# Optimization experiments

Measured on AMD Instinct MI355X. Metric: run time of the kernel, lower is better.

## Reference

```python
import jax, jax.numpy as jnp
import numpy as np

B, S, D = 2, 2048, 2048
NH, NKV, HD = 16, 4, 128
ROPE_BASE = 10000.0
NEG = -1e9


def _rope_tables(seq_len, dim):
    inv_freq = 1.0 / ROPE_BASE ** (jnp.arange(0, dim, 2, dtype=jnp.float32) / dim)
    t = jnp.arange(seq_len, dtype=jnp.float32)
    freqs = jnp.outer(t, inv_freq)                      # [S, dim/2]
    return jnp.cos(freqs), jnp.sin(freqs)


def _apply_rope(x, cos, sin):
    # x: [B, S, H, HD]; interleaved-pair rotation matching the original module
    x1 = x[..., ::2]
    x2 = x[..., 1::2]
    c = cos[None, :, None, :]
    s = sin[None, :, None, :]
    out1 = x1 * c - x2 * s
    out2 = x1 * s + x2 * c
    return jnp.stack([out1, out2], axis=-1).reshape(x.shape)


def setup_inputs() -> dict:
    key = jax.random.key(0)
    ks = jax.random.split(key, 5)
    x = jax.random.normal(ks[0], (B, S, D), dtype=jnp.float32)
    # causal additive mask [1, 1, S, S]
    causal = jnp.tril(jnp.ones((S, S), dtype=jnp.bool_))
    mask = jnp.where(causal, 0.0, NEG).astype(jnp.float32)[None, None]
    Wq = jax.random.normal(ks[1], (D, NH * HD), dtype=jnp.float32) * (D ** -0.5)
    Wk = jax.random.normal(ks[2], (D, NKV * HD), dtype=jnp.float32) * (D ** -0.5)
    Wv = jax.random.normal(ks[3], (D, NKV * HD), dtype=jnp.float32) * (D ** -0.5)
    Wo = jax.random.normal(ks[4], (NH * HD, D), dtype=jnp.float32) * ((NH * HD) ** -0.5)
    return {"x": x, "mask": mask, "Wq": Wq, "Wk": Wk, "Wv": Wv, "Wo": Wo}


def reference(x, mask, Wq, Wk, Wv, Wo):
    b, s, _ = x.shape
    q = (x @ Wq).reshape(b, s, NH, HD)
    k = (x @ Wk).reshape(b, s, NKV, HD)
    v = (x @ Wv).reshape(b, s, NKV, HD)

    cos, sin = _rope_tables(s, HD)
    q = _apply_rope(q, cos, sin)
    k = _apply_rope(k, cos, sin)

    rep = NH // NKV
    k = jnp.repeat(k, rep, axis=2)                       # [b, s, NH, HD]
    v = jnp.repeat(v, rep, axis=2)

    q = q.transpose(0, 2, 1, 3)                          # [b, NH, s, HD]
    k = k.transpose(0, 2, 1, 3)
    v = v.transpose(0, 2, 1, 3)

    scores = jnp.einsum('bhqd,bhkd->bhqk', q, k) / jnp.sqrt(jnp.float32(HD))
    scores = scores + mask
    attn = jax.nn.softmax(scores, axis=-1)
    out = jnp.einsum('bhqk,bhkd->bhqd', attn, v)
    out = out.transpose(0, 2, 1, 3).reshape(b, s, NH * HD)
    return out @ Wo
```

## Files before the change

### kernel.cpp

```cpp
#include <hip/hip_runtime.h>
#include <stdint.h>

#define B_    2
#define S_    2048
#define D_    2048
#define NH_   16
#define NKV_  4
#define HD_   128
#define M_    (B_*S_)
#define NQKV_ 3072

typedef __bf16 bf16x8 __attribute__((ext_vector_type(8)));
typedef float  f32x4  __attribute__((ext_vector_type(4)));

__device__ __forceinline__ unsigned short f2bf(float f) {
    unsigned int u = __float_as_uint(f);
    u += 0x7fffu + ((u >> 16) & 1u);
    return (unsigned short)(u >> 16);
}

__device__ __forceinline__ void async_cp16(const unsigned short* g, unsigned short* l) {
    __builtin_amdgcn_global_load_lds((const __attribute__((address_space(1))) void*)g,
                                     (__attribute__((address_space(3))) void*)l, 16, 0, 0);
}

__global__ void cast_x(const float* __restrict__ x, unsigned short* __restrict__ xb) {
    int idx = blockIdx.x * 256 + threadIdx.x;
    float4 v = ((const float4*)x)[idx];
    unsigned int lo = (unsigned int)f2bf(v.x) | ((unsigned int)f2bf(v.y) << 16);
    unsigned int hi = (unsigned int)f2bf(v.z) | ((unsigned int)f2bf(v.w) << 16);
    ((uint2*)xb)[idx] = make_uint2(lo, hi);
}

__global__ void transpose_cast(const float* __restrict__ src,
                               unsigned short* __restrict__ dst, int ncols) {
    __shared__ float tile[32][33];
    int tx = threadIdx.x, ty = threadIdx.y;
    int n0 = blockIdx.x * 32, k0 = blockIdx.y * 32;
#pragma unroll
    for (int i = 0; i < 4; i++) {
        int k = k0 + ty + i * 8;
        tile[ty + i * 8][tx] = src[(long)k * ncols + n0 + tx];
    }
    __syncthreads();
#pragma unroll
    for (int i = 0; i < 4; i++) {
        int n = n0 + ty + i * 8;
        dst[(long)n * 2048 + k0 + tx] = f2bf(tile[tx][ty + i * 8]);
    }
}

__global__ void rope_tables(float2* __restrict__ ctab) {
    int gid = blockIdx.x * 256 + threadIdx.x;
    int s = gid >> 6, i = gid & 63;
    float inv = exp2f(-(float)i * 0.20762050593046014f);
    float ang = (float)s * inv;
    float sn, cs; sincosf(ang, &sn, &cs);
    ctab[gid] = make_float2(cs, sn);
}

__global__ __launch_bounds__(256) void gemm_qkv(const unsigned short* __restrict__ A,
                                                const unsigned short* __restrict__ Bt,
                                                const float2* __restrict__ ctab,
                                                unsigned short* __restrict__ Qr,
                                                unsigned short* __restrict__ Kr,
                                                unsigned short* __restrict__ Vrow) {
    __shared__ unsigned short As[128 * 32];
    __shared__ unsigned short Bs[128 * 32];
    const int K = D_;
    const int bx = blockIdx.x, by = blockIdx.y;
    const int tid  = threadIdx.x;
    const int lane = tid & 63, wid = tid >> 6;
    const int quad = lane >> 4, l16 = lane & 15;
    const int wm = wid >> 1, wn = wid & 1;
    const int m0 = by * 128, n0 = bx * 128;
    f32x4 acc[4][4] = {};

    for (int k0 = 0; k0 < K; k0 += 32) {
        __syncthreads();
#pragma unroll
        for (int i = 0; i < 2; i++) {
            int gbase = (wid * 2 + i) * 64;
            int g = gbase + lane;
            int row = g >> 2, c = (g & 3) * 8;
            async_cp16(&A[(long)(m0 + row) * K + k0 + c], &As[gbase * 8]);
            async_cp16(&Bt[(long)(n0 + row) * K + k0 + c], &Bs[gbase * 8]);
        }
        __syncthreads();
        bf16x8 af[4], bfr[4];
#pragma unroll
        for (int mt = 0; mt < 4; mt++)
            af[mt] = *(const bf16x8*)&As[(wm * 64 + mt * 16 + l16) * 32 + quad * 8];
#pragma unroll
        for (int nt = 0; nt < 4; nt++)
            bfr[nt] = *(const bf16x8*)&Bs[(wn * 64 + nt * 16 + l16) * 32 + quad * 8];
#pragma unroll
        for (int mt = 0; mt < 4; mt++)
#pragma unroll
            for (int nt = 0; nt < 4; nt++)
                acc[mt][nt] = __builtin_amdgcn_mfma_f32_16x16x32_bf16(af[mt], bfr[nt], acc[mt][nt], 0, 0, 0);
    }

    if (bx < 20) {
#pragma unroll
        for (int mt = 0; mt < 4; mt++)
#pragma unroll
            for (int nt = 0; nt < 4; nt++)
#pragma unroll
                for (int r = 0; r < 4; r++) {
                    int row = m0 + wm * 64 + mt * 16 + quad * 4 + r;
                    int s = row & 2047, b = row >> 11;
                    int col = n0 + wn * 64 + nt * 16 + l16;
                    int d = col & 127;
                    float2 cs = ctab[s * 64 + (d >> 1)];
                    float own = acc[mt][nt][r];
                    float other = __shfl_xor(own, 1);
                    float val = (d & 1) ? (other * cs.y + own * cs.x)
                                        : (own * cs.x - other * cs.y);
                    if (col < 2048) {
                        int h = col >> 7;
                        Qr[(((long)(b * 16 + h) * 2048 + s) * 128) + d] = f2bf(val);
                    } else {
                        int kvh = (col - 2048) >> 7;
                        Kr[(((long)(b * 4 + kvh) * 2048 + s) * 128) + d] = f2bf(val);
                    }
                }
    } else {
#pragma unroll
        for (int mt = 0; mt < 4; mt++)
#pragma unroll
            for (int nt = 0; nt < 4; nt++)
#pragma unroll
                for (int r = 0; r < 4; r++) {
                    int row = m0 + wm * 64 + mt * 16 + quad * 4 + r;
                    int col = n0 + wn * 64 + nt * 16 + l16;
                    Vrow[(long)row * 512 + (col - 2560)] = f2bf(acc[mt][nt][r]);
                }
    }
}

__global__ __launch_bounds__(256) void gemm_bt(const unsigned short* __restrict__ A,
                                               const unsigned short* __restrict__ Bt,
                                               float* __restrict__ C, int N, int K) {
    __shared__ unsigned short As[128 * 32];
    __shared__ unsigned short Bs[128 * 32];
    const int bx = blockIdx.x, by = blockIdx.y;
    const int tid  = threadIdx.x;
    const int lane = tid & 63, wid = tid >> 6;
    const int quad = lane >> 4, l16 = lane & 15;
    const int wm = wid >> 1, wn = wid & 1;
    const int m0 = by * 128, n0 = bx * 128;
    f32x4 acc[4][4] = {};

    for (int k0 = 0; k0 < K; k0 += 32) {
        __syncthreads();
#pragma unroll
        for (int i = 0; i < 2; i++) {
            int gbase = (wid * 2 + i) * 64;
            int g = gbase + lane;
            int row = g >> 2, c = (g & 3) * 8;
            async_cp16(&A[(long)(m0 + row) * K + k0 + c], &As[gbase * 8]);
            async_cp16(&Bt[(long)(n0 + row) * K + k0 + c], &Bs[gbase * 8]);
        }
        __syncthreads();
        bf16x8 af[4], bfr[4];
#pragma unroll
        for (int mt = 0; mt < 4; mt++)
            af[mt] = *(const bf16x8*)&As[(wm * 64 + mt * 16 + l16) * 32 + quad * 8];
#pragma unroll
        for (int nt = 0; nt < 4; nt++)
            bfr[nt] = *(const bf16x8*)&Bs[(wn * 64 + nt * 16 + l16) * 32 + quad * 8];
#pragma unroll
        for (int mt = 0; mt < 4; mt++)
#pragma unroll
            for (int nt = 0; nt < 4; nt++)
                acc[mt][nt] = __builtin_amdgcn_mfma_f32_16x16x32_bf16(af[mt], bfr[nt], acc[mt][nt], 0, 0, 0);
    }
#pragma unroll
    for (int mt = 0; mt < 4; mt++)
#pragma unroll
        for (int nt = 0; nt < 4; nt++)
#pragma unroll
            for (int r = 0; r < 4; r++) {
                long row = m0 + wm * 64 + mt * 16 + quad * 4 + r;
                long col = n0 + wn * 64 + nt * 16 + l16;
                C[row * N + col] = acc[mt][nt][r];
            }
}

__global__ void v_trans_bf(const unsigned short* __restrict__ Vrow,
                           unsigned short* __restrict__ Vt) {
    __shared__ unsigned short tile[32][34];
    int tx = threadIdx.x, ty = threadIdx.y;
    int s0 = blockIdx.x * 32, d0 = blockIdx.y * 32;
    int bz = blockIdx.z;
    int b = bz >> 2, kvh = bz & 3;
#pragma unroll
    for (int i = 0; i < 4; i++) {
        int s = s0 + ty + i * 8;
        tile[ty + i * 8][tx] = Vrow[(long)(b * 2048 + s) * 512 + kvh * 128 + d0 + tx];
    }
    __syncthreads();
#pragma unroll
    for (int i = 0; i < 4; i++) {
        int d = d0 + ty + i * 8;
        Vt[((long)bz * 128 + d) * 2048 + s0 + tx] = tile[tx][ty + i * 8];
    }
}

__global__ __launch_bounds__(256) void attn_fwd(const unsigned short* __restrict__ Qr,
                                                const unsigned short* __restrict__ Kr,
                                                const unsigned short* __restrict__ Vt,
                                                unsigned short* __restrict__ O) {
    __shared__ unsigned short Ks[64][136];
    __shared__ unsigned short Vs[128][72];
    __shared__ unsigned short Ps[4][16][72];
    const int tid  = threadIdx.x;
    const int lane = tid & 63, wid = tid >> 6;
    const int quad = lane >> 4, l16 = lane & 15;
    const int pid = blockIdx.x, h = blockIdx.y, b = blockIdx.z;
    const int kvh = h >> 2;
    const unsigned short* qp = Qr + (long)(b * NH_ + h) * S_ * HD_;
    const unsigned short* kp = Kr + (long)(b * NKV_ + kvh) * S_ * HD_;
    const unsigned short* vp = Vt + (long)(b * NKV_ + kvh) * HD_ * S_;
    const float sc2 = 0.08838834764831845f * 1.4426950408889634f;

    bf16x8 ones;
#pragma unroll
    for (int i = 0; i < 8; i++) ones[i] = (__bf16)1.0f;

    for (int phase = 0; phase < 2; phase++) {
        const int qt = phase ? pid : 31 - pid;
        const int qw = qt * 64 + wid * 16;

        bf16x8 aq[4];
#pragma unroll
        for (int ks = 0; ks < 4; ks++)
            aq[ks] = *(const bf16x8*)&qp[(long)(qw + l16) * HD_ + ks * 32 + quad * 8];

        f32x4 o[8] = {};
        float mi[4], li[4];
#pragma unroll
        for (int r = 0; r < 4; r++) { mi[r] = -3.0e38f; li[r] = 0.f; }

        for (int kt = 0; kt <= qt; kt++) {
            const int kv0 = kt * 64;
            __syncthreads();
#pragma unroll
            for (int i = 0; i < 4; i++) {
                int idx = tid + i * 256;
                int row = idx >> 4, c = (idx & 15) * 8;
                *(uint4*)&Ks[row][c] = *(const uint4*)&kp[(long)(kv0 + row) * HD_ + c];
            }
#pragma unroll
            for (int i = 0; i < 4; i++) {
                int idx = tid + i * 256;
                int hd = idx >> 3, c = (idx & 7) * 8;
                *(uint4*)&Vs[hd][c] = *(const uint4*)&vp[(long)hd * S_ + kv0 + c];
            }
            __syncthreads();

            f32x4 s[4] = {};
#pragma unroll
            for (int ks = 0; ks < 4; ks++)
#pragma unroll
                for (int nt = 0; nt < 4; nt++) {
                    bf16x8 kb = *(const bf16x8*)&Ks[nt * 16 + l16][ks * 32 + quad * 8];
                    s[nt] = __builtin_amdgcn_mfma_f32_16x16x32_bf16(aq[ks], kb, s[nt], 0, 0, 0);
                }

            float mt[4];
#pragma unroll
            for (int r = 0; r < 4; r++) mt[r] = -3.0e38f;
            if (kv0 + 63 > qw) {
#pragma unroll
                for (int nt = 0; nt < 4; nt++) {
                    int kvp = kv0 + nt * 16 + l16;
#pragma unroll
                    for (int r = 0; r < 4; r++) {
                        float sv = s[nt][r] * sc2;
                        sv = (kvp <= qw + quad * 4 + r) ? sv : -1.0e30f;
                        s[nt][r] = sv;
                        mt[r] = fmaxf(mt[r], sv);
                    }
                }
            } else {
#pragma unroll
                for (int nt = 0; nt < 4; nt++)
#pragma unroll
                    for (int r = 0; r < 4; r++) {
                        float sv = s[nt][r] * sc2;
                        s[nt][r] = sv;
                        mt[r] = fmaxf(mt[r], sv);
                    }
            }
#pragma unroll
            for (int off = 1; off < 16; off <<= 1)
#pragma unroll
                for (int r = 0; r < 4; r++)
                    mt[r] = fmaxf(mt[r], __shfl_xor(mt[r], off));
            float al[4];
#pragma unroll
            for (int r = 0; r < 4; r++) {
                float mn = fmaxf(mi[r], mt[r]);
                al[r] = exp2f(mi[r] - mn);
                mi[r] = mn;
            }
#pragma unroll
            for (int nt = 0; nt < 4; nt++)
#pragma unroll
                for (int r = 0; r < 4; r++)
                    s[nt][r] = exp2f(s[nt][r] - mi[r]);
#pragma unroll
            for (int t = 0; t < 8; t++)
#pragma unroll
                for (int r = 0; r < 4; r++) o[t][r] *= al[r];

#pragma unroll
            for (int nt = 0; nt < 4; nt++)
#pragma unroll
                for (int r = 0; r < 4; r++)
                    Ps[wid][quad * 4 + r][nt * 16 + l16] = f2bf(s[nt][r]);

            f32x4 sumf = {};
#pragma unroll
            for (int ks2 = 0; ks2 < 2; ks2++) {
                bf16x8 pa = *(const bf16x8*)&Ps[wid][l16][ks2 * 32 + quad * 8];
                sumf = __builtin_amdgcn_mfma_f32_16x16x32_bf16(pa, ones, sumf, 0, 0, 0);
#pragma unroll
                for (int vt = 0; vt < 8; vt++) {
                    bf16x8 vb = *(const bf16x8*)&Vs[vt * 16 + l16][ks2 * 32 + quad * 8];
                    o[vt] = __builtin_amdgcn_mfma_f32_16x16x32_bf16(pa, vb, o[vt], 0, 0, 0);
                }
            }
#pragma unroll
            for (int r = 0; r < 4; r++) li[r] = li[r] * al[r] + sumf[r];
        }

#pragma unroll
        for (int r = 0; r < 4; r++) {
            float inv_l = 1.0f / li[r];
            int qpos = qw + quad * 4 + r;
#pragma unroll
            for (int vt = 0; vt < 8; vt++) {
                float val = o[vt][r] * inv_l;
                O[(long)(b * S_ + qpos) * 2048 + h * 128 + vt * 16 + l16] = f2bf(val);
            }
        }
    }
}

extern "C" void kernel_launch(void* const* d_in, const int* in_sizes, int n_in,
                              void* d_out, int out_size, void* d_ws, size_t ws_size,
                              hipStream_t stream) {
    const float* x  = (const float*)d_in[0];
    const float* Wq = (const float*)d_in[2];
    const float* Wk = (const float*)d_in[3];
    const float* Wv = (const float*)d_in[4];
    const float* Wo = (const float*)d_in[5];

    char* ws = (char*)d_ws;
    unsigned short* xb    = (unsigned short*)(ws);
    unsigned short* Wqkvt = (unsigned short*)(ws + 16777216);
    unsigned short* Wot   = (unsigned short*)(ws + 29360128);
    float2*         ctab  = (float2*)        (ws + 37748736);
    unsigned short* Qr    = (unsigned short*)(ws + 38797312);
    unsigned short* Kr    = (unsigned short*)(ws + 55574528);
    unsigned short* Vrow  = (unsigned short*)(ws + 59768832);
    unsigned short* Vt    = (unsigned short*)(ws + 63963136);
    unsigned short* attn  = (unsigned short*)(ws + 68157440);

    cast_x<<<8192, 256, 0, stream>>>(x, xb);
    dim3 tb(32, 8);
    transpose_cast<<<dim3(64, 64), tb, 0, stream>>>(Wq, Wqkvt, 2048);
    transpose_cast<<<dim3(16, 64), tb, 0, stream>>>(Wk, Wqkvt + 2048 * 2048, 512);
    transpose_cast<<<dim3(16, 64), tb, 0, stream>>>(Wv, Wqkvt + 2560 * 2048, 512);
    transpose_cast<<<dim3(64, 64), tb, 0, stream>>>(Wo, Wot, 2048);
    rope_tables<<<512, 256, 0, stream>>>(ctab);

    gemm_qkv<<<dim3(24, 32), 256, 0, stream>>>(xb, Wqkvt, ctab, Qr, Kr, Vrow);

    v_trans_bf<<<dim3(64, 4, 8), tb, 0, stream>>>(Vrow, Vt);

    attn_fwd<<<dim3(16, NH_, B_), 256, 0, stream>>>(Qr, Kr, Vt, attn);

    gemm_bt<<<dim3(16, 32), 256, 0, stream>>>(attn, Wot, (float*)d_out, D_, NH_ * HD_);
}
```

Baseline: 381.7 us.

## Replace 128x128 GEMMs with pipelined 256x256 tile core using swizzled LDS

Both the QKV projection and output projection GEMMs now use a shared 256x256-tile core with 8 waves and 128 KB of dynamic LDS. It prefetches K-halves asynchronously into quadrant buffers and issues MFMA clusters between barriers with raised wave priority. LDS addresses are XOR-swizzled to reduce bank conflicts. The goal is more reuse per loaded byte and overlap of global loads with matrix math. The cost is lower block count (192 and 128 blocks) and possible occupancy or tail-wave inefficiency on the CU count.

```diff
diff --git a/kernel.cpp b/kernel.cpp
--- a/kernel.cpp
+++ b/kernel.cpp
@@ -59,133 +59,270 @@
     ctab[gid] = make_float2(cs, sn);
 }
 
-__global__ __launch_bounds__(256) void gemm_qkv(const unsigned short* __restrict__ A,
-                                                const unsigned short* __restrict__ Bt,
-                                                const float2* __restrict__ ctab,
-                                                unsigned short* __restrict__ Qr,
-                                                unsigned short* __restrict__ Kr,
-                                                unsigned short* __restrict__ Vrow) {
-    __shared__ unsigned short As[128 * 32];
-    __shared__ unsigned short Bs[128 * 32];
-    const int K = D_;
-    const int bx = blockIdx.x, by = blockIdx.y;
+
+__device__ __forceinline__ bf16x8 lds_frag(const unsigned short* hb, int r, int ks, int quad) {
+    int p = (r * 128 + ks * 64 + quad * 16) ^ ((r & 4) << 3);
+    return *(const bf16x8*)((const char*)hb + p);
+}
+
+__device__ __forceinline__ void stage_half(const unsigned short* g, int Kel,
+                                           unsigned short* lhalf, int wid, int lane) {
+#pragma unroll
+    for (int i = 0; i < 2; i++) {
+        int chunk = wid * 2 + i;
+        int o = chunk * 1024 + lane * 16;
+        int row = o >> 7;
+        int cb = (o & 127) ^ ((row & 4) << 3);
+        async_cp16((const unsigned short*)((const char*)g + (size_t)row * Kel * 2 + cb),
+                   lhalf + chunk * 512);
+    }
+}
+
+template<int MB, int NB>
+__device__ __forceinline__ void cluster(f32x4 (*acc)[4], bf16x8 (*a)[2], bf16x8 (*b)[2]) {
+    __builtin_amdgcn_sched_barrier(0);
+    __builtin_amdgcn_s_barrier();
+    asm volatile("s_waitcnt lgkmcnt(0)" ::: "memory");
+    __builtin_amdgcn_sched_barrier(0);
+    __builtin_amdgcn_s_setprio(1);
+#pragma unroll
+    for (int ks = 0; ks < 2; ks++)
+#pragma unroll
+        for (int mi = 0; mi < 4; mi++)
+#pragma unroll
+            for (int ni = 0; ni < 2; ni++)
+                acc[MB + mi][NB + ni] = __builtin_amdgcn_mfma_f32_16x16x32_bf16(
+                    a[mi][ks], b[ni][ks], acc[MB + mi][NB + ni], 0, 0, 0);
+    __builtin_amdgcn_s_setprio(0);
+    __builtin_amdgcn_sched_barrier(0);
+    __builtin_amdgcn_s_barrier();
+    __builtin_amdgcn_sched_barrier(0);
+}
+
+__device__ __forceinline__ void gemm256_core(const unsigned short* __restrict__ A,
+                                             const unsigned short* __restrict__ Bt,
+                                             const int K, const int m0, const int n0,
+                                             char* sm, f32x4 (*acc)[4]) {
     const int tid  = threadIdx.x;
     const int lane = tid & 63, wid = tid >> 6;
     const int quad = lane >> 4, l16 = lane & 15;
-    const int wm = wid >> 1, wn = wid & 1;
-    const int m0 = by * 128, n0 = bx * 128;
-    f32x4 acc[4][4] = {};
-
-    for (int k0 = 0; k0 < K; k0 += 32) {
-        __syncthreads();
-#pragma unroll
-        for (int i = 0; i < 2; i++) {
-            int gbase = (wid * 2 + i) * 64;
-            int g = gbase + lane;
-            int row = g >> 2, c = (g & 3) * 8;
-            async_cp16(&A[(long)(m0 + row) * K + k0 + c], &As[gbase * 8]);
-            async_cp16(&Bt[(long)(n0 + row) * K + k0 + c], &Bs[gbase * 8]);
-        }
-        __syncthreads();
-        bf16x8 af[4], bfr[4];
-#pragma unroll
-        for (int mt = 0; mt < 4; mt++)
-            af[mt] = *(const bf16x8*)&As[(wm * 64 + mt * 16 + l16) * 32 + quad * 8];
-#pragma unroll
-        for (int nt = 0; nt < 4; nt++)
-            bfr[nt] = *(const bf16x8*)&Bs[(wn * 64 + nt * 16 + l16) * 32 + quad * 8];
-#pragma unroll
-        for (int mt = 0; mt < 4; mt++)
-#pragma unroll
-            for (int nt = 0; nt < 4; nt++)
-                acc[mt][nt] = __builtin_amdgcn_mfma_f32_16x16x32_bf16(af[mt], bfr[nt], acc[mt][nt], 0, 0, 0);
-    }
-
-    if (bx < 20) {
-#pragma unroll
-        for (int mt = 0; mt < 4; mt++)
-#pragma unroll
-            for (int nt = 0; nt < 4; nt++)
+    const int wm = wid >> 2, wn = wid & 3;
+
+    unsigned short* sA00 = (unsigned short*)(sm);
+    unsigned short* sA01 = (unsigned short*)(sm + 16384);
+    unsigned short* sA10 = (unsigned short*)(sm + 32768);
+    unsigned short* sA11 = (unsigned short*)(sm + 49152);
+    unsigned short* sB00 = (unsigned short*)(sm + 65536);
+    unsigned short* sB01 = (unsigned short*)(sm + 81920);
+    unsigned short* sB10 = (unsigned short*)(sm + 98304);
+    unsigned short* sB11 = (unsigned short*)(sm + 114688);
+
+    const unsigned short* A0 = A  + (size_t)m0 * K;
+    const unsigned short* A1 = A  + (size_t)(m0 + 128) * K;
+    const unsigned short* B0 = Bt + (size_t)n0 * K;
+    const unsigned short* B1 = Bt + (size_t)(n0 + 128) * K;
+
+    stage_half(A0,      K, sA00, wid, lane);
+    stage_half(B1,      K, sB01, wid, lane);
+    stage_half(A1,      K, sA01, wid, lane);
+    stage_half(B0,      K, sB00, wid, lane);
+    __builtin_amdgcn_sched_barrier(0);
+    stage_half(A0 + 64, K, sA10, wid, lane);
+    stage_half(B1 + 64, K, sB11, wid, lane);
+    stage_half(A1 + 64, K, sA11, wid, lane);
+    asm volatile("s_waitcnt vmcnt(6)" ::: "memory");
+    __builtin_amdgcn_sched_barrier(0);
+    __builtin_amdgcn_s_barrier();
+    __builtin_amdgcn_sched_barrier(0);
+
+    const int NIT = K >> 7;
+    for (int j = 0; j < NIT; ++j) {
+        const bool st = (j < NIT - 1);
+        const int kof1 = (2 * j + 1) * 64;
+        const int kof2 = (2 * j + 2) * 64;
+        const int kof3 = (2 * j + 3) * 64;
+        bf16x8 af[4][2], bA[2][2], bB[2][2];
+
+#pragma unroll
+        for (int mi = 0; mi < 4; mi++)
+#pragma unroll
+            for (int ks = 0; ks < 2; ks++)
+                af[mi][ks] = lds_frag(sA00, wm * 64 + mi * 16 + l16, ks, quad);
+#pragma unroll
+        for (int ni = 0; ni < 2; ni++)
+#pragma unroll
+            for (int ks = 0; ks < 2; ks++)
+                bA[ni][ks] = lds_frag(sB00, wn * 32 + ni * 16 + l16, ks, quad);
+        stage_half(B0 + kof1, K, sB10, wid, lane);
+        cluster<0, 0>(acc, af, bA);
+
+#pragma unroll
+        for (int ni = 0; ni < 2; ni++)
+#pragma unroll
+            for (int ks = 0; ks < 2; ks++)
+                bB[ni][ks] = lds_frag(sB01, wn * 32 + ni * 16 + l16, ks, quad);
+        if (st) stage_half(A0 + kof2, K, sA00, wid, lane);
+        cluster<0, 2>(acc, af, bB);
+
+#pragma unroll
+        for (int mi = 0; mi < 4; mi++)
+#pragma unroll
+            for (int ks = 0; ks < 2; ks++)
+                af[mi][ks] = lds_frag(sA01, wm * 64 + mi * 16 + l16, ks, quad);
+        if (st) stage_half(B1 + kof2, K, sB01, wid, lane);
+        cluster<4, 2>(acc, af, bB);
+
+#pragma unroll
+        for (int ni = 0; ni < 2; ni++)
+#pragma unroll
+            for (int ks = 0; ks < 2; ks++)
+                bA[ni][ks] = lds_frag(sB00, wn * 32 + ni * 16 + l16, ks, quad);
+        if (st) {
+            stage_half(A1 + kof2, K, sA01, wid, lane);
+            asm volatile("s_waitcnt vmcnt(6)" ::: "memory");
+        } else {
+            asm volatile("s_waitcnt vmcnt(0)" ::: "memory");
+        }
+        cluster<4, 0>(acc, af, bA);
+
+#pragma unroll
+        for (int mi = 0; mi < 4; mi++)
+#pragma unroll
+            for (int ks = 0; ks < 2; ks++)
+                af[mi][ks] = lds_frag(sA10, wm * 64 + mi * 16 + l16, ks, quad);
+#pragma unroll
+        for (int ni = 0; ni < 2; ni++)
+#pragma unroll
+            for (int ks = 0; ks < 2; ks++)
+                bA[ni][ks] = lds_frag(sB10, wn * 32 + ni * 16 + l16, ks, quad);
+        if (st) stage_half(B0 + kof2, K, sB00, wid, lane);
+        cluster<0, 0>(acc, af, bA);
+
+#pragma unroll
+        for (int ni = 0; ni < 2; ni++)
+#pragma unroll
+            for (int ks = 0; ks < 2; ks++)
+                bB[ni][ks] = lds_frag(sB11, wn * 32 + ni * 16 + l16, ks, quad);
+        if (st) stage_half(A0 + kof3, K, sA10, wid, lane);
+        cluster<0, 2>(acc, af, bB);
+
+#pragma unroll
+        for (int mi = 0; mi < 4; mi++)
+#pragma unroll
+            for (int ks = 0; ks < 2; ks++)
+                af[mi][ks] = lds_frag(sA11, wm * 64 + mi * 16 + l16, ks, quad);
+        if (st) stage_half(B1 + kof3, K, sB11, wid, lane);
+        cluster<4, 2>(acc, af, bB);
+
+#pragma unroll
+        for (int ni = 0; ni < 2; ni++)
+#pragma unroll
+            for (int ks = 0; ks < 2; ks++)
+                bA[ni][ks] = lds_frag(sB10, wn * 32 + ni * 16 + l16, ks, quad);
+        if (st) {
+            stage_half(A1 + kof3, K, sA11, wid, lane);
+            asm volatile("s_waitcnt vmcnt(6)" ::: "memory");
+        }
+        cluster<4, 0>(acc, af, bA);
+    }
+}
+
+__global__ __launch_bounds__(512, 2) void gemm_qkv256(const unsigned short* __restrict__ A,
+                                                      const unsigned short* __restrict__ Bt,
+                                                      const float2* __restrict__ ctab,
+                                                      unsigned short* __restrict__ Qr,
+                                                      unsigned short* __restrict__ Kr,
+                                                      unsigned short* __restrict__ Vrow) {
+    extern __shared__ char sm[];
+    const int m0 = blockIdx.y * 256, n0 = blockIdx.x * 256;
+    f32x4 acc[8][4] = {};
+    gemm256_core(A, Bt, D_, m0, n0, sm, acc);
+
+    const int tid  = threadIdx.x;
+    const int lane = tid & 63, wid = tid >> 6;
+    const int quad = lane >> 4, l16 = lane & 15;
+    const int wm = wid >> 2, wn = wid & 3;
+
+    if (n0 < 2048) {
+#pragma unroll
+        for (int mt = 0; mt < 8; mt++) {
+            int rowb = m0 + ((mt & 4) << 5) + wm * 64 + (mt & 3) * 16 + quad * 4;
+#pragma unroll
+            for (int nt = 0; nt < 4; nt++) {
+                int col = n0 + ((nt & 2) << 6) + wn * 32 + (nt & 1) * 16 + l16;
+                int h = col >> 7, d = col & 127;
 #pragma unroll
                 for (int r = 0; r < 4; r++) {
-                    int row = m0 + wm * 64 + mt * 16 + quad * 4 + r;
+                    int row = rowb + r;
                     int s = row & 2047, b = row >> 11;
-                    int col = n0 + wn * 64 + nt * 16 + l16;
-                    int d = col & 127;
                     float2 cs = ctab[s * 64 + (d >> 1)];
                     float own = acc[mt][nt][r];
                     float other = __shfl_xor(own, 1);
                     float val = (d & 1) ? (other * cs.y + own * cs.x)
                                         : (own * cs.x - other * cs.y);
-                    if (col < 2048) {
-                        int h = col >> 7;
-                        Qr[(((long)(b * 16 + h) * 2048 + s) * 128) + d] = f2bf(val);
-                    } else {
-                        int kvh = (col - 2048) >> 7;
-                        Kr[(((long)(b * 4 + kvh) * 2048 + s) * 128) + d] = f2bf(val);
-                    }
+                    Qr[((size_t)(b * 16 + h) * 2048 + s) * 128 + d] = f2bf(val);
                 }
+            }
+        }
+    } else if (n0 < 2560) {
+#pragma unroll
+        for (int mt = 0; mt < 8; mt++) {
+            int rowb = m0 + ((mt & 4) << 5) + wm * 64 + (mt & 3) * 16 + quad * 4;
+#pragma unroll
+            for (int nt = 0; nt < 4; nt++) {
+                int col = n0 + ((nt & 2) << 6) + wn * 32 + (nt & 1) * 16 + l16;
+                int kvh = (col - 2048) >> 7, d = col & 127;
+#pragma unroll
+                for (int r = 0; r < 4; r++) {
+                    int row = rowb + r;
+                    int s = row & 2047, b = row >> 11;
+                    float2 cs = ctab[s * 64 + (d >> 1)];
+                    float own = acc[mt][nt][r];
+                    float other = __shfl_xor(own, 1);
+                    float val = (d & 1) ? (other * cs.y + own * cs.x)
+                                        : (own * cs.x - other * cs.y);
+                    Kr[((size_t)(b * 4 + kvh) * 2048 + s) * 128 + d] = f2bf(val);
+                }
+            }
+        }
     } else {
 #pragma unroll
-        for (int mt = 0; mt < 4; mt++)
-#pragma unroll
-            for (int nt = 0; nt < 4; nt++)
-#pragma unroll
-                for (int r = 0; r < 4; r++) {
-                    int row = m0 + wm * 64 + mt * 16 + quad * 4 + r;
-                    int col = n0 + wn * 64 + nt * 16 + l16;
-                    Vrow[(long)row * 512 + (col - 2560)] = f2bf(acc[mt][nt][r]);
-                }
-    }
-}
-
-__global__ __launch_bounds__(256) void gemm_bt(const unsigned short* __restrict__ A,
-                                               const unsigned short* __restrict__ Bt,
-                                               float* __restrict__ C, int N, int K) {
-    __shared__ unsigned short As[128 * 32];
-    __shared__ unsigned short Bs[128 * 32];
-    const int bx = blockIdx.x, by = blockIdx.y;
+        for (int mt = 0; mt < 8; mt++) {
+            int rowb = m0 + ((mt & 4) << 5) + wm * 64 + (mt & 3) * 16 + quad * 4;
+#pragma unroll
+            for (int nt = 0; nt < 4; nt++) {
+                int col = n0 + ((nt & 2) << 6) + wn * 32 + (nt & 1) * 16 + l16;
+#pragma unroll
+                for (int r = 0; r < 4; r++)
+                    Vrow[(size_t)(rowb + r) * 512 + (col - 2560)] = f2bf(acc[mt][nt][r]);
+            }
+        }
+    }
+}
+
+__global__ __launch_bounds__(512, 2) void gemm_bt256(const unsigned short* __restrict__ A,
+                                                     const unsigned short* __restrict__ Bt,
+                                                     float* __restrict__ C) {
+    extern __shared__ char sm[];
+    const int m0 = blockIdx.y * 256, n0 = blockIdx.x * 256;
+    f32x4 acc[8][4] = {};
+    gemm256_core(A, Bt, NH_ * HD_, m0, n0, sm, acc);
+
     const int tid  = threadIdx.x;
     const int lane = tid & 63, wid = tid >> 6;
     const int quad = lane >> 4, l16 = lane & 15;
-    const int wm = wid >> 1, wn = wid & 1;
-    const int m0 = by * 128, n0 = bx * 128;
-    f32x4 acc[4][4] = {};
-
-    for (int k0 = 0; k0 < K; k0 += 32) {
-        __syncthreads();
-#pragma unroll
-        for (int i = 0; i < 2; i++) {
-            int gbase = (wid * 2 + i) * 64;
-            int g = gbase + lane;
-            int row = g >> 2, c = (g & 3) * 8;
-            async_cp16(&A[(long)(m0 + row) * K + k0 + c], &As[gbase * 8]);
-            async_cp16(&Bt[(long)(n0 + row) * K + k0 + c], &Bs[gbase * 8]);
-        }
-        __syncthreads();
-        bf16x8 af[4], bfr[4];
-#pragma unroll
-        for (int mt = 0; mt < 4; mt++)
-            af[mt] = *(const bf16x8*)&As[(wm * 64 + mt * 16 + l16) * 32 + quad * 8];
-#pragma unroll
-        for (int nt = 0; nt < 4; nt++)
-            bfr[nt] = *(const bf16x8*)&Bs[(wn * 64 + nt * 16 + l16) * 32 + quad * 8];
-#pragma unroll
-        for (int mt = 0; mt < 4; mt++)
-#pragma unroll
-            for (int nt = 0; nt < 4; nt++)
-                acc[mt][nt] = __builtin_amdgcn_mfma_f32_16x16x32_bf16(af[mt], bfr[nt], acc[mt][nt], 0, 0, 0);
-    }
-#pragma unroll
-    for (int mt = 0; mt < 4; mt++)
-#pragma unroll
-        for (int nt = 0; nt < 4; nt++)
-#pragma unroll
-            for (int r = 0; r < 4; r++) {
-                long row = m0 + wm * 64 + mt * 16 + quad * 4 + r;
-                long col = n0 + wn * 64 + nt * 16 + l16;
-                C[row * N + col] = acc[mt][nt][r];
-            }
+    const int wm = wid >> 2, wn = wid & 3;
+#pragma unroll
+    for (int mt = 0; mt < 8; mt++) {
+        int rowb = m0 + ((mt & 4) << 5) + wm * 64 + (mt & 3) * 16 + quad * 4;
+#pragma unroll
+        for (int nt = 0; nt < 4; nt++) {
+            int col = n0 + ((nt & 2) << 6) + wn * 32 + (nt & 1) * 16 + l16;
+#pragma unroll
+            for (int r = 0; r < 4; r++)
+                C[(size_t)(rowb + r) * 2048 + col] = acc[mt][nt][r];
+        }
+    }
 }
 
 __global__ void v_trans_bf(const unsigned short* __restrict__ Vrow,
@@ -370,6 +507,15 @@
     unsigned short* Vt    = (unsigned short*)(ws + 63963136);
     unsigned short* attn  = (unsigned short*)(ws + 68157440);
 
+    static int attr_set = 0;
+    if (!attr_set) {
+        hipFuncSetAttribute(reinterpret_cast<const void*>(gemm_qkv256),
+                            hipFuncAttributeMaxDynamicSharedMemorySize, 131072);
+        hipFuncSetAttribute(reinterpret_cast<const void*>(gemm_bt256),
+                            hipFuncAttributeMaxDynamicSharedMemorySize, 131072);
+        attr_set = 1;
+    }
+
     cast_x<<<8192, 256, 0, stream>>>(x, xb);
     dim3 tb(32, 8);
     transpose_cast<<<dim3(64, 64), tb, 0, stream>>>(Wq, Wqkvt, 2048);
@@ -378,11 +524,11 @@
     transpose_cast<<<dim3(64, 64), tb, 0, stream>>>(Wo, Wot, 2048);
     rope_tables<<<512, 256, 0, stream>>>(ctab);
 
-    gemm_qkv<<<dim3(24, 32), 256, 0, stream>>>(xb, Wqkvt, ctab, Qr, Kr, Vrow);
+    gemm_qkv256<<<dim3(12, 16), 512, 131072, stream>>>(xb, Wqkvt, ctab, Qr, Kr, Vrow);
 
     v_trans_bf<<<dim3(64, 4, 8), tb, 0, stream>>>(Vrow, Vt);
 
     attn_fwd<<<dim3(16, NH_, B_), 256, 0, stream>>>(Qr, Kr, Vt, attn);
 
-    gemm_bt<<<dim3(16, 32), 256, 0, stream>>>(attn, Wot, (float*)d_out, D_, NH_ * HD_);
-}
+    gemm_bt256<<<dim3(8, 16), 512, 131072, stream>>>(attn, Wot, (float*)d_out);
+}
```

After: 369.9 us. 3.1% less time.
